# Kernel tuning notes

Hardware: AMD Instinct MI355X
Metric: run time of the kernel (lower is better)

The kernel has to match this reference:

```python
import jax, jax.numpy as jnp
import numpy as np

GRAPH_SIZE = 96
ROWS = 5
COLS = 4
BATCH = 2048


def setup_inputs() -> dict:
    key = jax.random.key(0)
    k1, k2 = jax.random.split(key)
    x = jax.random.normal(k1, (BATCH, GRAPH_SIZE, GRAPH_SIZE), dtype=jnp.float32)
    # coef: nn.Parameter zeros -> kaiming_normal_, i.e. N(0, sqrt(2/fan_in)), fan_in=COLS
    coef = jax.random.normal(k2, (ROWS, COLS), dtype=jnp.float32) * np.float32(np.sqrt(2.0 / COLS))
    return {"x": x, "coef": coef}


def _acoef(x, coef):
    """Batched version of ACoef.forward.

    Per sample: t_i = trace(x^(i+2)) for i in [0, rows); scalar out =
    sum_{i,j} coef[i,j] * t_i^(j+1) / (G*G)^(i+j+1).
    """
    rows, cols = coef.shape
    G = x.shape[-1]
    xr = x.reshape(-1, G, G)  # [B, G, G]
    a = jnp.matmul(xr, xr)    # x^2 == a_series[0]
    traces = []
    for i in range(rows):
        traces.append(jnp.einsum('bii->b', a))  # trace(x^(i+2))
        if i < rows - 1:
            a = jnp.matmul(xr, a)  # advance to x^(i+3)
    t = jnp.stack(traces, axis=1)  # [B, rows]
    numel = jnp.float32(G * G)
    jexp = jnp.arange(1, cols + 1, dtype=jnp.float32)  # j+1
    iexp = jnp.arange(rows, dtype=jnp.float32)         # i
    denom = numel ** (iexp[:, None] + jexp[None, :])   # numel^(i+j+1), [rows, cols]
    ret = (t[:, :, None] ** jexp[None, None, :]) / denom  # [B, rows, cols]
    return jnp.sum(coef[None, :, :] * ret, axis=(1, 2))   # [B]


def reference(x, coef):
    return _acoef(x, coef)
```

## Files before the change

### kernel.cpp

```cpp
#include <hip/hip_runtime.h>
#include <stdint.h>

#define G 96
#define GS (G*G)
#define ST 104
#define ARR (G*ST)
#define NT 256

typedef short bf16x8  __attribute__((ext_vector_type(8)));
typedef short short4v __attribute__((ext_vector_type(4)));
typedef float f32x4   __attribute__((ext_vector_type(4)));

__device__ __forceinline__ short f2bf(float f) {
  uint32_t u = __builtin_bit_cast(uint32_t, f);
  u += 0x7FFFu + ((u >> 16) & 1u);
  return (short)(u >> 16);
}
__device__ __forceinline__ float bf2f(short s) {
  uint32_t u = ((uint32_t)(uint16_t)s) << 16;
  return __builtin_bit_cast(float, u);
}

__device__ __forceinline__ void mm_phase(const short* __restrict__ P,
                                         const short* __restrict__ Q,
                                         int wm, int wn, int lr, int lq,
                                         f32x4 acc[3][3]) {
  #pragma unroll
  for (int ks = 0; ks < 3; ++ks) {
    const int k0 = ks*32 + lq*8;
    bf16x8 af[3], bg[3];
    #pragma unroll
    for (int i = 0; i < 3; ++i)
      af[i] = *reinterpret_cast<const bf16x8*>(&P[(wm + i*16 + lr)*ST + k0]);
    #pragma unroll
    for (int j = 0; j < 3; ++j)
      bg[j] = *reinterpret_cast<const bf16x8*>(&Q[(wn + j*16 + lr)*ST + k0]);
    #pragma unroll
    for (int i = 0; i < 3; ++i)
      #pragma unroll
      for (int j = 0; j < 3; ++j)
        acc[i][j] = __builtin_amdgcn_mfma_f32_16x16x32_bf16(af[i], bg[j], acc[i][j], 0, 0, 0);
  }
}

__global__ __launch_bounds__(NT, 4) void acoef_kernel(
    const float* __restrict__ x, const float* __restrict__ coef,
    float* __restrict__ out) {
  __shared__ short sm[2*ARR];
  __shared__ float red[4][8];

  short* X  = sm;
  short* R1 = sm + ARR;

  const int tid  = threadIdx.x;
  const int b    = blockIdx.x;
  const int lane = tid & 63;
  const int w    = tid >> 6;
  const int wm   = (w >> 1) * 48;
  const int wn   = (w & 1)  * 48;
  const int lr   = lane & 15;
  const int lq   = lane >> 4;
  const int cr0  = lq * 4;

  const float* xg = x + (size_t)b * GS;
  #pragma unroll
  for (int it = 0; it < 9; ++it) {
    int f = tid + it*NT;
    float4 v = reinterpret_cast<const float4*>(xg)[f];
    int row = f / 24, c4 = (f - row*24) * 4;
    short4v sv = {f2bf(v.x), f2bf(v.y), f2bf(v.z), f2bf(v.w)};
    *reinterpret_cast<short4v*>(&X[row*ST + c4]) = sv;
  }
  __syncthreads();

  #pragma unroll
  for (int it = 0; it < 9; ++it) {
    int u  = tid + it*NT;
    int r2 = u % 96, cb = (u / 96) * 4;
    short4v sv = { X[(cb+0)*ST + r2], X[(cb+1)*ST + r2],
                   X[(cb+2)*ST + r2], X[(cb+3)*ST + r2] };
    *reinterpret_cast<short4v*>(&R1[r2*ST + cb]) = sv;
  }
  __syncthreads();

  f32x4 acc[3][3];
  #pragma unroll
  for (int i=0;i<3;i++)
    #pragma unroll
    for (int j=0;j<3;j++) acc[i][j] = (f32x4){0.f,0.f,0.f,0.f};
  mm_phase(X, R1, wm, wn, lr, lq, acc);

  float t0 = 0.f;
  #pragma unroll
  for (int i = 0; i < 3; ++i)
    #pragma unroll
    for (int j = 0; j < 3; ++j) {
      const int row0 = wm + i*16 + cr0, col = wn + j*16 + lr;
      #pragma unroll
      for (int r = 0; r < 4; ++r)
        if (row0 + r == col) t0 += acc[i][j][r];
    }
  __syncthreads();

  #pragma unroll
  for (int i = 0; i < 3; ++i)
    #pragma unroll
    for (int j = 0; j < 3; ++j) {
      const int row0 = wm + i*16 + cr0, col = wn + j*16 + lr;
      short4v sv = {f2bf(acc[i][j][0]), f2bf(acc[i][j][1]),
                    f2bf(acc[i][j][2]), f2bf(acc[i][j][3])};
      *reinterpret_cast<short4v*>(&R1[col*ST + row0]) = sv;
    }
  __syncthreads();

  f32x4 a2[3][3];
  #pragma unroll
  for (int i=0;i<3;i++)
    #pragma unroll
    for (int j=0;j<3;j++) a2[i][j] = (f32x4){0.f,0.f,0.f,0.f};
  mm_phase(R1, X, wm, wn, lr, lq, a2);

  float t1=0.f, t2=0.f, t3=0.f, t4=0.f;
  #pragma unroll
  for (int i = 0; i < 3; ++i)
    #pragma unroll
    for (int j = 0; j < 3; ++j) {
      const int row0 = wm + i*16 + cr0, col = wn + j*16 + lr;
      short4v ar = *reinterpret_cast<const short4v*>(&R1[col*ST + row0]);
      #pragma unroll
      for (int r = 0; r < 4; ++r) {
        float wv = a2[i][j][r];
        if (row0 + r == col) t1 += wv;
        t2 += wv * bf2f(X[(row0+r)*ST + col]);
        t3 += wv * bf2f(ar[r]);
      }
    }
  __syncthreads();

  #pragma unroll
  for (int i = 0; i < 3; ++i)
    #pragma unroll
    for (int j = 0; j < 3; ++j) {
      const int row0 = wm + i*16 + cr0, col = wn + j*16 + lr;
      short4v sv = {f2bf(a2[i][j][0]), f2bf(a2[i][j][1]),
                    f2bf(a2[i][j][2]), f2bf(a2[i][j][3])};
      *reinterpret_cast<short4v*>(&R1[col*ST + row0]) = sv;
    }
  __syncthreads();

  #pragma unroll
  for (int i = 0; i < 3; ++i)
    #pragma unroll
    for (int j = 0; j < 3; ++j) {
      const int row0 = wm + i*16 + cr0, col = wn + j*16 + lr;
      #pragma unroll
      for (int r = 0; r < 4; ++r)
        t4 += a2[i][j][r] * bf2f(R1[(row0+r)*ST + col]);
    }

  #pragma unroll
  for (int off = 32; off > 0; off >>= 1) {
    t0 += __shfl_down(t0, off, 64);
    t1 += __shfl_down(t1, off, 64);
    t2 += __shfl_down(t2, off, 64);
    t3 += __shfl_down(t3, off, 64);
    t4 += __shfl_down(t4, off, 64);
  }
  if (lane == 0) {
    red[w][0]=t0; red[w][1]=t1; red[w][2]=t2; red[w][3]=t3; red[w][4]=t4;
  }
  __syncthreads();
  if (tid == 0) {
    float T[5];
    #pragma unroll
    for (int k = 0; k < 5; ++k) T[k] = red[0][k]+red[1][k]+red[2][k]+red[3][k];
    const float inv = 1.0f / (float)GS;
    float o = 0.f, pi = 1.f;
    #pragma unroll
    for (int i = 0; i < 5; ++i) {
      float u = T[i] * inv;
      float up = u;
      #pragma unroll
      for (int j = 0; j < 4; ++j) { o += coef[i*4+j] * up * pi; up *= u; }
      pi *= inv;
    }
    out[b] = o;
  }
}

extern "C" void kernel_launch(void* const* d_in, const int* in_sizes, int n_in,
                              void* d_out, int out_size, void* d_ws, size_t ws_size,
                              hipStream_t stream) {
  const float* x    = (const float*)d_in[0];
  const float* coef = (const float*)d_in[1];
  float* out        = (float*)d_out;
  const int batch   = in_sizes[0] / GS;
  acoef_kernel<<<batch, NT, 0, stream>>>(x, coef, out);
}
```

Baseline: 28.69 us.

## Process two batch samples per block to interleave independent MFMA chains

Each block now handles two samples, with doubled shared memory. It runs each phase for both samples back to back, so independent MFMA and LDS work can overlap and the per-phase barriers are shared. Occupancy drops from 4 to 2 blocks per CU via launch bounds, and register pressure roughly doubles for the accumulators. Coef is staged in shared memory, and the launch assumes an even batch.

```diff
diff --git a/kernel.cpp b/kernel.cpp
--- a/kernel.cpp
+++ b/kernel.cpp
@@ -43,14 +43,20 @@
   }
 }
 
-__global__ __launch_bounds__(NT, 4) void acoef_kernel(
+#define ZERO9(A) do { \
+  _Pragma("unroll") for (int i_=0;i_<3;i_++) \
+    _Pragma("unroll") for (int j_=0;j_<3;j_++) A[i_][j_] = (f32x4){0.f,0.f,0.f,0.f}; \
+} while (0)
+
+__global__ __launch_bounds__(NT, 2) void acoef_kernel(
     const float* __restrict__ x, const float* __restrict__ coef,
     float* __restrict__ out) {
-  __shared__ short sm[2*ARR];
-  __shared__ float red[4][8];
-
-  short* X  = sm;
-  short* R1 = sm + ARR;
+  __shared__ short sm[4*ARR];
+  __shared__ float red[4][10];
+  __shared__ float cf[20];
+
+  short* Xp[2]  = { sm,           sm + 2*ARR };
+  short* R1p[2] = { sm + ARR,     sm + 3*ARR };
 
   const int tid  = threadIdx.x;
   const int b    = blockIdx.x;
@@ -62,118 +68,148 @@
   const int lq   = lane >> 4;
   const int cr0  = lq * 4;
 
-  const float* xg = x + (size_t)b * GS;
-  #pragma unroll
-  for (int it = 0; it < 9; ++it) {
-    int f = tid + it*NT;
-    float4 v = reinterpret_cast<const float4*>(xg)[f];
-    int row = f / 24, c4 = (f - row*24) * 4;
-    short4v sv = {f2bf(v.x), f2bf(v.y), f2bf(v.z), f2bf(v.w)};
-    *reinterpret_cast<short4v*>(&X[row*ST + c4]) = sv;
-  }
-  __syncthreads();
-
-  #pragma unroll
-  for (int it = 0; it < 9; ++it) {
-    int u  = tid + it*NT;
-    int r2 = u % 96, cb = (u / 96) * 4;
-    short4v sv = { X[(cb+0)*ST + r2], X[(cb+1)*ST + r2],
-                   X[(cb+2)*ST + r2], X[(cb+3)*ST + r2] };
-    *reinterpret_cast<short4v*>(&R1[r2*ST + cb]) = sv;
-  }
-  __syncthreads();
-
-  f32x4 acc[3][3];
-  #pragma unroll
-  for (int i=0;i<3;i++)
-    #pragma unroll
-    for (int j=0;j<3;j++) acc[i][j] = (f32x4){0.f,0.f,0.f,0.f};
-  mm_phase(X, R1, wm, wn, lr, lq, acc);
-
-  float t0 = 0.f;
-  #pragma unroll
-  for (int i = 0; i < 3; ++i)
-    #pragma unroll
-    for (int j = 0; j < 3; ++j) {
-      const int row0 = wm + i*16 + cr0, col = wn + j*16 + lr;
-      #pragma unroll
-      for (int r = 0; r < 4; ++r)
-        if (row0 + r == col) t0 += acc[i][j][r];
+  if (tid < 20) cf[tid] = coef[tid];
+
+  #pragma unroll
+  for (int s = 0; s < 2; ++s) {
+    const float* xg = x + (size_t)(2*b + s) * GS;
+    short* X = Xp[s];
+    #pragma unroll
+    for (int it = 0; it < 9; ++it) {
+      int f = tid + it*NT;
+      float4 v = reinterpret_cast<const float4*>(xg)[f];
+      int row = f / 24, c4 = (f - row*24) * 4;
+      short4v sv = {f2bf(v.x), f2bf(v.y), f2bf(v.z), f2bf(v.w)};
+      *reinterpret_cast<short4v*>(&X[row*ST + c4]) = sv;
     }
-  __syncthreads();
-
-  #pragma unroll
-  for (int i = 0; i < 3; ++i)
-    #pragma unroll
-    for (int j = 0; j < 3; ++j) {
-      const int row0 = wm + i*16 + cr0, col = wn + j*16 + lr;
-      short4v sv = {f2bf(acc[i][j][0]), f2bf(acc[i][j][1]),
-                    f2bf(acc[i][j][2]), f2bf(acc[i][j][3])};
-      *reinterpret_cast<short4v*>(&R1[col*ST + row0]) = sv;
+  }
+  __syncthreads();
+
+  #pragma unroll
+  for (int s = 0; s < 2; ++s) {
+    short* X = Xp[s]; short* R1 = R1p[s];
+    #pragma unroll
+    for (int it = 0; it < 9; ++it) {
+      int u  = tid + it*NT;
+      int r2 = u % 96, cb = (u / 96) * 4;
+      short4v sv = { X[(cb+0)*ST + r2], X[(cb+1)*ST + r2],
+                     X[(cb+2)*ST + r2], X[(cb+3)*ST + r2] };
+      *reinterpret_cast<short4v*>(&R1[r2*ST + cb]) = sv;
     }
-  __syncthreads();
-
-  f32x4 a2[3][3];
-  #pragma unroll
-  for (int i=0;i<3;i++)
-    #pragma unroll
-    for (int j=0;j<3;j++) a2[i][j] = (f32x4){0.f,0.f,0.f,0.f};
-  mm_phase(R1, X, wm, wn, lr, lq, a2);
-
-  float t1=0.f, t2=0.f, t3=0.f, t4=0.f;
-  #pragma unroll
-  for (int i = 0; i < 3; ++i)
-    #pragma unroll
-    for (int j = 0; j < 3; ++j) {
-      const int row0 = wm + i*16 + cr0, col = wn + j*16 + lr;
-      short4v ar = *reinterpret_cast<const short4v*>(&R1[col*ST + row0]);
-      #pragma unroll
-      for (int r = 0; r < 4; ++r) {
-        float wv = a2[i][j][r];
-        if (row0 + r == col) t1 += wv;
-        t2 += wv * bf2f(X[(row0+r)*ST + col]);
-        t3 += wv * bf2f(ar[r]);
-      }
-    }
-  __syncthreads();
-
-  #pragma unroll
-  for (int i = 0; i < 3; ++i)
-    #pragma unroll
-    for (int j = 0; j < 3; ++j) {
-      const int row0 = wm + i*16 + cr0, col = wn + j*16 + lr;
-      short4v sv = {f2bf(a2[i][j][0]), f2bf(a2[i][j][1]),
-                    f2bf(a2[i][j][2]), f2bf(a2[i][j][3])};
-      *reinterpret_cast<short4v*>(&R1[col*ST + row0]) = sv;
-    }
-  __syncthreads();
-
-  #pragma unroll
-  for (int i = 0; i < 3; ++i)
-    #pragma unroll
-    for (int j = 0; j < 3; ++j) {
-      const int row0 = wm + i*16 + cr0, col = wn + j*16 + lr;
-      #pragma unroll
-      for (int r = 0; r < 4; ++r)
-        t4 += a2[i][j][r] * bf2f(R1[(row0+r)*ST + col]);
-    }
+  }
+  __syncthreads();
+
+  float tt[2][5];
+  #pragma unroll
+  for (int s = 0; s < 2; ++s)
+    #pragma unroll
+    for (int k = 0; k < 5; ++k) tt[s][k] = 0.f;
+
+  f32x4 acc1[2][3][3];
+  #pragma unroll
+  for (int s = 0; s < 2; ++s) {
+    ZERO9(acc1[s]);
+    mm_phase(Xp[s], R1p[s], wm, wn, lr, lq, acc1[s]);
+    #pragma unroll
+    for (int i = 0; i < 3; ++i)
+      #pragma unroll
+      for (int j = 0; j < 3; ++j) {
+        const int row0 = wm + i*16 + cr0, col = wn + j*16 + lr;
+        #pragma unroll
+        for (int r = 0; r < 4; ++r)
+          if (row0 + r == col) tt[s][0] += acc1[s][i][j][r];
+      }
+  }
+  __syncthreads();
+
+  #pragma unroll
+  for (int s = 0; s < 2; ++s) {
+    short* R1 = R1p[s];
+    #pragma unroll
+    for (int i = 0; i < 3; ++i)
+      #pragma unroll
+      for (int j = 0; j < 3; ++j) {
+        const int row0 = wm + i*16 + cr0, col = wn + j*16 + lr;
+        short4v sv = {f2bf(acc1[s][i][j][0]), f2bf(acc1[s][i][j][1]),
+                      f2bf(acc1[s][i][j][2]), f2bf(acc1[s][i][j][3])};
+        *reinterpret_cast<short4v*>(&R1[col*ST + row0]) = sv;
+      }
+  }
+  __syncthreads();
+
+  f32x4 acc2[2][3][3];
+  #pragma unroll
+  for (int s = 0; s < 2; ++s) {
+    ZERO9(acc2[s]);
+    mm_phase(R1p[s], Xp[s], wm, wn, lr, lq, acc2[s]);
+    short* X = Xp[s]; short* R1 = R1p[s];
+    #pragma unroll
+    for (int i = 0; i < 3; ++i)
+      #pragma unroll
+      for (int j = 0; j < 3; ++j) {
+        const int row0 = wm + i*16 + cr0, col = wn + j*16 + lr;
+        short4v ar = *reinterpret_cast<const short4v*>(&R1[col*ST + row0]);
+        #pragma unroll
+        for (int r = 0; r < 4; ++r) {
+          float wv = acc2[s][i][j][r];
+          if (row0 + r == col) tt[s][1] += wv;
+          tt[s][2] += wv * bf2f(X[(row0+r)*ST + col]);
+          tt[s][3] += wv * bf2f(ar[r]);
+        }
+      }
+  }
+  __syncthreads();
+
+  #pragma unroll
+  for (int s = 0; s < 2; ++s) {
+    short* R1 = R1p[s];
+    #pragma unroll
+    for (int i = 0; i < 3; ++i)
+      #pragma unroll
+      for (int j = 0; j < 3; ++j) {
+        const int row0 = wm + i*16 + cr0, col = wn + j*16 + lr;
+        short4v sv = {f2bf(acc2[s][i][j][0]), f2bf(acc2[s][i][j][1]),
+                      f2bf(acc2[s][i][j][2]), f2bf(acc2[s][i][j][3])};
+        *reinterpret_cast<short4v*>(&R1[col*ST + row0]) = sv;
+      }
+  }
+  __syncthreads();
+
+  #pragma unroll
+  for (int s = 0; s < 2; ++s) {
+    short* R1 = R1p[s];
+    #pragma unroll
+    for (int i = 0; i < 3; ++i)
+      #pragma unroll
+      for (int j = 0; j < 3; ++j) {
+        const int row0 = wm + i*16 + cr0, col = wn + j*16 + lr;
+        #pragma unroll
+        for (int r = 0; r < 4; ++r)
+          tt[s][4] += acc2[s][i][j][r] * bf2f(R1[(row0+r)*ST + col]);
+      }
+  }
 
   #pragma unroll
   for (int off = 32; off > 0; off >>= 1) {
-    t0 += __shfl_down(t0, off, 64);
-    t1 += __shfl_down(t1, off, 64);
-    t2 += __shfl_down(t2, off, 64);
-    t3 += __shfl_down(t3, off, 64);
-    t4 += __shfl_down(t4, off, 64);
+    #pragma unroll
+    for (int s = 0; s < 2; ++s)
+      #pragma unroll
+      for (int k = 0; k < 5; ++k)
+        tt[s][k] += __shfl_down(tt[s][k], off, 64);
   }
   if (lane == 0) {
-    red[w][0]=t0; red[w][1]=t1; red[w][2]=t2; red[w][3]=t3; red[w][4]=t4;
-  }
-  __syncthreads();
-  if (tid == 0) {
+    #pragma unroll
+    for (int s = 0; s < 2; ++s)
+      #pragma unroll
+      for (int k = 0; k < 5; ++k) red[w][s*5+k] = tt[s][k];
+  }
+  __syncthreads();
+  if (tid < 2) {
+    const int s = tid;
     float T[5];
     #pragma unroll
-    for (int k = 0; k < 5; ++k) T[k] = red[0][k]+red[1][k]+red[2][k]+red[3][k];
+    for (int k = 0; k < 5; ++k)
+      T[k] = red[0][s*5+k]+red[1][s*5+k]+red[2][s*5+k]+red[3][s*5+k];
     const float inv = 1.0f / (float)GS;
     float o = 0.f, pi = 1.f;
     #pragma unroll
@@ -181,10 +217,10 @@
       float u = T[i] * inv;
       float up = u;
       #pragma unroll
-      for (int j = 0; j < 4; ++j) { o += coef[i*4+j] * up * pi; up *= u; }
+      for (int j = 0; j < 4; ++j) { o += cf[i*4+j] * up * pi; up *= u; }
       pi *= inv;
     }
-    out[b] = o;
+    out[2*b + s] = o;
   }
 }
 
@@ -195,5 +231,5 @@
   const float* coef = (const float*)d_in[1];
   float* out        = (float*)d_out;
   const int batch   = in_sizes[0] / GS;
-  acoef_kernel<<<batch, NT, 0, stream>>>(x, coef, out);
-}
+  acoef_kernel<<<batch/2, NT, 0, stream>>>(x, coef, out);
+}
```

Result: slower. 32.86 us (+14.5%).
